# Kernel tuning notes

Hardware: AMD Instinct MI355X
Metric: run time of the kernel (lower is better)

The kernel has to match this reference:

```python
import jax, jax.numpy as jnp
import numpy as np

B, C, H, W = 8, 512, 32, 32
NUM_HEADS, D_K = 8, 64
EPS = 1e-5


def setup_inputs() -> dict:
    key = jax.random.key(0)
    ks = jax.random.split(key, 6)
    s = 1.0 / np.sqrt(C)
    return {
        "x": jax.random.normal(ks[0], (B, C, H, W), dtype=jnp.float32),
        "wq": jax.random.uniform(ks[1], (C, NUM_HEADS * D_K), jnp.float32, -s, s),
        "bq": jnp.zeros((NUM_HEADS * D_K,), jnp.float32),
        "wk": jax.random.uniform(ks[2], (C, NUM_HEADS * D_K), jnp.float32, -s, s),
        "bk": jnp.zeros((NUM_HEADS * D_K,), jnp.float32),
        "wv": jax.random.uniform(ks[3], (C, NUM_HEADS * D_K), jnp.float32, -s, s),
        "bv": jnp.zeros((NUM_HEADS * D_K,), jnp.float32),
        "ln_g": jnp.ones((C,), jnp.float32),
        "ln_b": jnp.zeros((C,), jnp.float32),
        "wo": jax.random.uniform(ks[4], (NUM_HEADS * D_K, C), jnp.float32, -s, s),
        "bo": jnp.zeros((C,), jnp.float32),
    }


def reference(x, wq, bq, wk, bk, wv, bv, ln_g, ln_b, wo, bo):
    b, c, h, w = x.shape
    seq = h * w
    # [B, C, H, W] -> [B, S, C]
    t = x.reshape(b, c, seq).transpose(0, 2, 1)
    residual = t
    # LayerNorm over channel dim
    mu = jnp.mean(t, axis=-1, keepdims=True)
    var = jnp.var(t, axis=-1, keepdims=True)
    tn = (t - mu) * jax.lax.rsqrt(var + EPS) * ln_g + ln_b
    # QKV projections -> [B, S, h, d]
    q = (tn @ wq + bq).reshape(b, seq, NUM_HEADS, D_K)
    k = (tn @ wk + bk).reshape(b, seq, NUM_HEADS, D_K)
    v = (tn @ wv + bv).reshape(b, seq, NUM_HEADS, D_K)
    scores = jnp.einsum("bqhd,bkhd->bhqk", q, k) / np.sqrt(D_K).astype(np.float32)
    attn = jax.nn.softmax(scores, axis=-1)
    out = jnp.einsum("bhqk,bkhd->bqhd", attn, v).reshape(b, seq, NUM_HEADS * D_K)
    out = out @ wo + bo
    return out + residual
```

## Files before the change

kernel.cpp:

```cpp
#include <hip/hip_runtime.h>
#include <hip/hip_bf16.h>
#include <stdint.h>

#define BB 8
#define CC 512
#define SS 1024
#define NH 8
#define DK 64
#define MM (BB*SS)
#define PQ 72

typedef __attribute__((ext_vector_type(8))) short bf16x8;
typedef __attribute__((ext_vector_type(4))) float f32x4;

__device__ inline float b2f(unsigned short u) {
    union { unsigned int i; float f; } x; x.i = ((unsigned int)u) << 16; return x.f;
}
__device__ inline unsigned short f2b(float f) {
    union { float f; unsigned int i; } x; x.f = f;
    unsigned int r = (x.i + 0x7FFFu + ((x.i >> 16) & 1u)) >> 16;
    return (unsigned short)r;
}
__device__ inline unsigned int cvtpk(float lo, float hi) {
    unsigned int r;
    asm("v_cvt_pk_bf16_f32 %0, %1, %2" : "=v"(r) : "v"(lo), "v"(hi));
    return r;
}
__device__ inline f32x4 mfma16(bf16x8 a, bf16x8 b, f32x4 c) {
    return __builtin_amdgcn_mfma_f32_16x16x32_bf16(a, b, c, 0, 0, 0);
}
__device__ __forceinline__ void gload16(const void* g, void* l) {
    __builtin_amdgcn_global_load_lds(
        (const __attribute__((address_space(1))) void*)g,
        (__attribute__((address_space(3))) void*)l, 16, 0, 0);
}

__global__ void __launch_bounds__(256) wtrans_kernel(const float* __restrict__ wq,
                                                     const float* __restrict__ wk,
                                                     const float* __restrict__ wv,
                                                     const float* __restrict__ wo,
                                                     unsigned short* __restrict__ wT) {
    __shared__ float lds[64][65];
    const float* w = (blockIdx.z == 0) ? wq : (blockIdx.z == 1) ? wk : (blockIdx.z == 2) ? wv : wo;
    unsigned short* o = wT + (size_t)blockIdx.z * (512 * 512);
    const int n0 = blockIdx.x * 64, k0 = blockIdx.y * 64;
    const int t = threadIdx.x;
    {
        const int nl = (t & 15) * 4, kr = t >> 4;
#pragma unroll
        for (int i = 0; i < 4; ++i) {
            float4 v = *(const float4*)(w + (size_t)(k0 + kr + i * 16) * 512 + n0 + nl);
            lds[kr + i * 16][nl] = v.x; lds[kr + i * 16][nl + 1] = v.y;
            lds[kr + i * 16][nl + 2] = v.z; lds[kr + i * 16][nl + 3] = v.w;
        }
    }
    __syncthreads();
    {
        const int k8 = (t & 7) * 8, nr = t >> 3;
#pragma unroll
        for (int ii = 0; ii < 2; ++ii) {
            int n = nr + ii * 32;
            unsigned short pk[8];
#pragma unroll
            for (int e = 0; e < 8; ++e) pk[e] = f2b(lds[k8 + e][n]);
            *(uint4*)&o[(size_t)(n0 + n) * 512 + k0 + k8] = *(uint4*)pk;
        }
    }
}

__global__ void __launch_bounds__(256) stats_kernel(const float* __restrict__ x,
                                                    float2* __restrict__ stats) {
    __shared__ float2 red[16][17];
    const int b = blockIdx.y, s0 = blockIdx.x * 16;
    const int sl = threadIdx.x & 15, cg = threadIdx.x >> 4;
    const float* xp = x + ((size_t)b * 512 + cg * 32) * 1024 + s0 + sl;
    float sum = 0.f, sq = 0.f;
#pragma unroll 8
    for (int i = 0; i < 32; ++i) { float v = xp[(size_t)i * 1024]; sum += v; sq += v * v; }
    red[cg][sl] = make_float2(sum, sq);
    __syncthreads();
    if (threadIdx.x < 16) {
        float s = 0.f, q = 0.f;
#pragma unroll
        for (int c = 0; c < 16; ++c) { s += red[c][threadIdx.x].x; q += red[c][threadIdx.x].y; }
        float mean = s * (1.f / 512.f);
        float var = q * (1.f / 512.f) - mean * mean;
        stats[b * 1024 + s0 + threadIdx.x] = make_float2(mean, rsqrtf(var + 1e-5f));
    }
}

__global__ void __launch_bounds__(256) xln_kernel(const float* __restrict__ x,
                                                  const float2* __restrict__ stats,
                                                  const float* __restrict__ g,
                                                  const float* __restrict__ bta,
                                                  unsigned short* __restrict__ xt,
                                                  unsigned short* __restrict__ tn) {
    __shared__ float lds[64][65];
    const int s0 = blockIdx.x * 64, c0 = blockIdx.y * 64, b = blockIdx.z;
    const int t = threadIdx.x;
    {
        const int sl = (t & 15) * 4, cr = t >> 4;
#pragma unroll
        for (int i = 0; i < 4; ++i) {
            float4 v = *(const float4*)(x + ((size_t)b * 512 + c0 + cr + i * 16) * 1024 + s0 + sl);
            lds[cr + i * 16][sl] = v.x; lds[cr + i * 16][sl + 1] = v.y;
            lds[cr + i * 16][sl + 2] = v.z; lds[cr + i * 16][sl + 3] = v.w;
        }
    }
    __syncthreads();
    {
        const int c8 = (t & 7) * 8, sr = t >> 3;
        float gg[8], bb[8];
        {
            float4 g0 = *(const float4*)(g + c0 + c8), g1 = *(const float4*)(g + c0 + c8 + 4);
            float4 b0 = *(const float4*)(bta + c0 + c8), b1 = *(const float4*)(bta + c0 + c8 + 4);
            gg[0]=g0.x; gg[1]=g0.y; gg[2]=g0.z; gg[3]=g0.w; gg[4]=g1.x; gg[5]=g1.y; gg[6]=g1.z; gg[7]=g1.w;
            bb[0]=b0.x; bb[1]=b0.y; bb[2]=b0.z; bb[3]=b0.w; bb[4]=b1.x; bb[5]=b1.y; bb[6]=b1.z; bb[7]=b1.w;
        }
#pragma unroll
        for (int ii = 0; ii < 2; ++ii) {
            int s = sr + ii * 32;
            float2 st = stats[b * 1024 + s0 + s];
            unsigned short rawp[8], nrmp[8];
#pragma unroll
            for (int e = 0; e < 8; ++e) {
                float v = lds[c8 + e][s];
                rawp[e] = f2b(v);
                nrmp[e] = f2b((v - st.x) * st.y * gg[e] + bb[e]);
            }
            *(uint4*)&xt[((size_t)b * 1024 + s0 + s) * 512 + c0 + c8] = *(uint4*)rawp;
            *(uint4*)&tn[((size_t)b * 1024 + s0 + s) * 512 + c0 + c8] = *(uint4*)nrmp;
        }
    }
}

__device__ inline void gemm_tile(const unsigned short* __restrict__ A,
                                 const unsigned short* __restrict__ Bt,
                                 int m0, int n0,
                                 unsigned short (*A_lds)[128 * 64],
                                 unsigned short (*B_lds)[128 * 64],
                                 f32x4 acc[4][4]) {
    const int t = threadIdx.x;
    const int lane = t & 63, w = t >> 6;
    const int l15 = lane & 15, l4 = lane >> 4;
    const int wm = (w >> 1) * 64, wn = (w & 1) * 64;
    auto STAGE = [&](int bi, int kt) {
#pragma unroll
        for (int i = 0; i < 4; ++i) {
            int chunk = i * 256 + t;
            int row = chunk >> 3, kc = (chunk & 7) * 8;
            gload16(A + (size_t)(m0 + row) * 512 + kt * 64 + kc, &A_lds[bi][chunk * 8]);
            gload16(Bt + (size_t)(n0 + row) * 512 + kt * 64 + kc, &B_lds[bi][chunk * 8]);
        }
    };
    STAGE(0, 0);
    __syncthreads();
#pragma unroll 1
    for (int kt = 0; kt < 8; ++kt) {
        const int bi = kt & 1;
        if (kt < 7) STAGE(bi ^ 1, kt + 1);
#pragma unroll
        for (int kk = 0; kk < 2; ++kk) {
            bf16x8 af[4], bfr[4];
#pragma unroll
            for (int i = 0; i < 4; ++i)
                af[i] = *(const bf16x8*)&A_lds[bi][(wm + i * 16 + l15) * 64 + kk * 32 + l4 * 8];
#pragma unroll
            for (int j = 0; j < 4; ++j)
                bfr[j] = *(const bf16x8*)&B_lds[bi][(wn + j * 16 + l15) * 64 + kk * 32 + l4 * 8];
#pragma unroll
            for (int i = 0; i < 4; ++i)
#pragma unroll
                for (int j = 0; j < 4; ++j)
                    acc[i][j] = mfma16(af[i], bfr[j], acc[i][j]);
        }
        __syncthreads();
    }
}

__global__ void __launch_bounds__(256) gemm_qkv_kernel(const unsigned short* __restrict__ tn,
                                                       const unsigned short* __restrict__ wT,
                                                       const float* __restrict__ bq,
                                                       const float* __restrict__ bk,
                                                       const float* __restrict__ bv,
                                                       unsigned short* __restrict__ outbase) {
    __shared__ alignas(16) unsigned short A_lds[2][128 * 64];
    __shared__ alignas(16) unsigned short B_lds[2][128 * 64];
    const int z = blockIdx.z;
    const unsigned short* Bt = wT + (size_t)z * (512 * 512);
    const float* bias = (z == 0) ? bq : (z == 1) ? bk : bv;
    const int m0 = blockIdx.x * 128, n0 = blockIdx.y * 128;
    f32x4 acc[4][4];
    const f32x4 z4 = {0.f, 0.f, 0.f, 0.f};
#pragma unroll
    for (int i = 0; i < 4; ++i)
#pragma unroll
        for (int j = 0; j < 4; ++j) acc[i][j] = z4;
    gemm_tile(tn, Bt, m0, n0, A_lds, B_lds, acc);
    const int lane = threadIdx.x & 63, w = threadIdx.x >> 6;
    const int l15 = lane & 15, l4 = lane >> 4;
    const int wm = (w >> 1) * 64, wn = (w & 1) * 64;
    if (z < 2) {
        unsigned short* out = outbase + (size_t)z * MM * 512;
#pragma unroll
        for (int i = 0; i < 4; ++i)
#pragma unroll
            for (int j = 0; j < 4; ++j) {
                int col = n0 + wn + j * 16 + l15;
                float bcol = bias[col];
#pragma unroll
                for (int r = 0; r < 4; ++r) {
                    int row = m0 + wm + i * 16 + l4 * 4 + r;
                    out[(size_t)row * 512 + col] = f2b(acc[i][j][r] + bcol);
                }
            }
    } else {
        unsigned short* vt = outbase + (size_t)2 * MM * 512;
#pragma unroll
        for (int i = 0; i < 4; ++i)
#pragma unroll
            for (int j = 0; j < 4; ++j) {
                int col = n0 + wn + j * 16 + l15;
                float bcol = bias[col];
                int rowb = m0 + wm + i * 16 + l4 * 4;
                int bi = rowb >> 10, s0 = rowb & 1023;
                uint2 pk;
                pk.x = (unsigned int)f2b(acc[i][j][0] + bcol) |
                       ((unsigned int)f2b(acc[i][j][1] + bcol) << 16);
                pk.y = (unsigned int)f2b(acc[i][j][2] + bcol) |
                       ((unsigned int)f2b(acc[i][j][3] + bcol) << 16);
                *(uint2*)&vt[((size_t)bi * 512 + col) * 1024 + s0] = pk;
            }
    }
}

__global__ void __launch_bounds__(256) attn_kernel(const unsigned short* __restrict__ q,
                                                   const unsigned short* __restrict__ k,
                                                   const unsigned short* __restrict__ vt,
                                                   unsigned short* __restrict__ o) {
    __shared__ alignas(16) unsigned short Kl[2][64 * 64];
    __shared__ alignas(16) unsigned short Vl[2][64 * 64];
    __shared__ alignas(16) unsigned short Pl[4][16 * PQ];
    const int qt = blockIdx.x, h = blockIdx.y, b = blockIdx.z;
    const int t = threadIdx.x, lane = t & 63, w = t >> 6;
    const int l15 = lane & 15, l4 = lane >> 4;

    const float QSC = 0.125f * 1.44269504f;
    const int qrow = qt * 64 + w * 16 + l15;
    const unsigned short* qp = q + ((size_t)(b * SS + qrow)) * 512 + h * 64;
    bf16x8 qf[2];
#pragma unroll
    for (int kk = 0; kk < 2; ++kk) {
        bf16x8 tmp = *(const bf16x8*)(qp + kk * 32 + l4 * 8);
#pragma unroll
        for (int e = 0; e < 8; ++e)
            tmp[e] = (short)f2b(b2f((unsigned short)tmp[e]) * QSC);
        qf[kk] = tmp;
    }

    const unsigned short* krow_base = k + ((size_t)(b * SS)) * 512 + h * 64;
    const unsigned short* vrow_base = vt + ((size_t)(b * NH + h) * DK) * SS;

    auto STAGE = [&](int bi, int kt) {
        const int key0 = kt * 64;
#pragma unroll
        for (int i = 0; i < 2; ++i) {
            int chunk = i * 256 + t;
            int row = chunk >> 3;
            int scb = ((chunk & 7) * 16) ^ ((row & 7) << 4);
            gload16((const char*)(krow_base + (size_t)(key0 + row) * 512) + scb,
                    &Kl[bi][chunk * 8]);
            gload16((const char*)(vrow_base + (size_t)row * SS + key0) + scb,
                    &Vl[bi][chunk * 8]);
        }
    };

    float m_run = -1e30f, l_run = 0.f;
    f32x4 acc_o[4];
    const f32x4 z4 = {0.f, 0.f, 0.f, 0.f};
#pragma unroll
    for (int j = 0; j < 4; ++j) acc_o[j] = z4;

    STAGE(0, 0);
    __syncthreads();

#pragma unroll 1
    for (int kt = 0; kt < 16; ++kt) {
        const int bi = kt & 1;
        if (kt < 15) STAGE(bi ^ 1, kt + 1);

        f32x4 sc[4];
#pragma unroll
        for (int j = 0; j < 4; ++j) sc[j] = z4;
        __builtin_amdgcn_s_setprio(1);
#pragma unroll
        for (int kk = 0; kk < 2; ++kk)
#pragma unroll
            for (int j = 0; j < 4; ++j) {
                int row = j * 16 + l15;
                int cb = (kk * 64 + l4 * 16) ^ ((row & 7) << 4);
                bf16x8 kf = *(const bf16x8*)((const char*)Kl[bi] + row * 128 + cb);
                sc[j] = mfma16(kf, qf[kk], sc[j]);
            }
        __builtin_amdgcn_s_setprio(0);

        float mx = fmaxf(fmaxf(sc[0][0], sc[0][1]), fmaxf(sc[0][2], sc[0][3]));
#pragma unroll
        for (int j = 1; j < 4; ++j)
            mx = fmaxf(mx, fmaxf(fmaxf(sc[j][0], sc[j][1]), fmaxf(sc[j][2], sc[j][3])));

        if (!__all(mx - m_run <= 8.f)) {
            mx = fmaxf(mx, __shfl_xor(mx, 16));
            mx = fmaxf(mx, __shfl_xor(mx, 32));
            float mnew = fmaxf(m_run, mx);
            float scl = exp2f(m_run - mnew);
            m_run = mnew;
            l_run *= scl;
            float scl_r[4];
#pragma unroll
            for (int r = 0; r < 4; ++r) scl_r[r] = __shfl(scl, (l4 << 2) | r);
#pragma unroll
            for (int j = 0; j < 4; ++j)
#pragma unroll
                for (int r = 0; r < 4; ++r) acc_o[j][r] *= scl_r[r];
        }

        float p[4][4], lsum = 0.f;
#pragma unroll
        for (int j = 0; j < 4; ++j)
#pragma unroll
            for (int r = 0; r < 4; ++r) {
                p[j][r] = exp2f(sc[j][r] - m_run);
                lsum += p[j][r];
            }
        l_run += lsum;

#pragma unroll
        for (int j = 0; j < 4; ++j) {
            uint2 pk;
            pk.x = cvtpk(p[j][0], p[j][1]);
            pk.y = cvtpk(p[j][2], p[j][3]);
            *(uint2*)&Pl[w][l15 * PQ + j * 16 + l4 * 4] = pk;
        }

        __builtin_amdgcn_s_setprio(1);
#pragma unroll
        for (int kk = 0; kk < 2; ++kk) {
            bf16x8 pf = *(const bf16x8*)&Pl[w][l15 * PQ + kk * 32 + l4 * 8];
#pragma unroll
            for (int j = 0; j < 4; ++j) {
                int row = j * 16 + l15;
                int cb = (kk * 64 + l4 * 16) ^ ((row & 7) << 4);
                bf16x8 vf = *(const bf16x8*)((const char*)Vl[bi] + row * 128 + cb);
                acc_o[j] = mfma16(pf, vf, acc_o[j]);
            }
        }
        __builtin_amdgcn_s_setprio(0);

        __syncthreads();
    }

    float l_tot = l_run;
    l_tot += __shfl_xor(l_tot, 16);
    l_tot += __shfl_xor(l_tot, 32);
    float l_r[4];
#pragma unroll
    for (int r = 0; r < 4; ++r) l_r[r] = __shfl(l_tot, (l4 << 2) | r);

#pragma unroll
    for (int j = 0; j < 4; ++j)
#pragma unroll
        for (int r = 0; r < 4; ++r) {
            int row = qt * 64 + w * 16 + l4 * 4 + r;
            float val = acc_o[j][r] / l_r[r];
            o[((size_t)(b * SS + row)) * 512 + h * 64 + j * 16 + l15] = f2b(val);
        }
}

__global__ void __launch_bounds__(256) gemm_out_kernel(const unsigned short* __restrict__ ao,
                                                       const unsigned short* __restrict__ woT,
                                                       const float* __restrict__ bo,
                                                       const unsigned short* __restrict__ xt,
                                                       float* __restrict__ out) {
    __shared__ alignas(16) unsigned short A_lds[2][128 * 64];
    __shared__ alignas(16) unsigned short B_lds[2][128 * 64];
    const int m0 = blockIdx.x * 128, n0 = blockIdx.y * 128;
    f32x4 acc[4][4];
    const f32x4 z4 = {0.f, 0.f, 0.f, 0.f};
#pragma unroll
    for (int i = 0; i < 4; ++i)
#pragma unroll
        for (int j = 0; j < 4; ++j) acc[i][j] = z4;
    gemm_tile(ao, woT, m0, n0, A_lds, B_lds, acc);
    const int lane = threadIdx.x & 63, w = threadIdx.x >> 6;
    const int l15 = lane & 15, l4 = lane >> 4;
    const int wm = (w >> 1) * 64, wn = (w & 1) * 64;
#pragma unroll
    for (int i = 0; i < 4; ++i)
#pragma unroll
        for (int j = 0; j < 4; ++j) {
            int col = n0 + wn + j * 16 + l15;
            float bcol = bo[col];
#pragma unroll
            for (int r = 0; r < 4; ++r) {
                int row = m0 + wm + i * 16 + l4 * 4 + r;
                float resid = b2f(xt[(size_t)row * 512 + col]);
                out[(size_t)row * 512 + col] = acc[i][j][r] + bcol + resid;
            }
        }
}

extern "C" void kernel_launch(void* const* d_in, const int* in_sizes, int n_in,
                              void* d_out, int out_size, void* d_ws, size_t ws_size,
                              hipStream_t stream) {
    const float* x   = (const float*)d_in[0];
    const float* wq  = (const float*)d_in[1];
    const float* bq  = (const float*)d_in[2];
    const float* wk  = (const float*)d_in[3];
    const float* bk  = (const float*)d_in[4];
    const float* wv  = (const float*)d_in[5];
    const float* bv  = (const float*)d_in[6];
    const float* lng = (const float*)d_in[7];
    const float* lnb = (const float*)d_in[8];
    const float* wo  = (const float*)d_in[9];
    const float* bo  = (const float*)d_in[10];
    float* out = (float*)d_out;

    unsigned short* ws  = (unsigned short*)d_ws;
    const size_t M1 = (size_t)1024 * 1024;
    unsigned short* tn   = ws;
    unsigned short* qkvb = ws + 4 * M1;
    unsigned short* wT   = ws + 16 * M1;
    unsigned short* xt   = ws + 17 * M1;
    unsigned short* ao   = tn;
    float2* stats = (float2*)qkvb;

    wtrans_kernel<<<dim3(8, 8, 4), 256, 0, stream>>>(wq, wk, wv, wo, wT);
    stats_kernel<<<dim3(64, 8), 256, 0, stream>>>(x, stats);
    xln_kernel<<<dim3(16, 8, 8), 256, 0, stream>>>(x, stats, lng, lnb, xt, tn);
    gemm_qkv_kernel<<<dim3(64, 4, 3), 256, 0, stream>>>(tn, wT, bq, bk, bv, qkvb);
    attn_kernel<<<dim3(16, 8, 8), 256, 0, stream>>>(qkvb,
                                                    qkvb + (size_t)MM * 512,
                                                    qkvb + (size_t)2 * MM * 512,
                                                    ao);
    gemm_out_kernel<<<dim3(64, 4), 256, 0, stream>>>(ao, wT + (size_t)3 * 512 * 512, bo, xt, out);
}
```

Baseline: 188.2 us.

## Load attention K/V fragments directly to registers, remap blocks to XCDs, vectorize stats

The attention kernel stops staging K and V tiles through shared memory with a block-wide barrier. Each wave now loads its own K and V MFMA fragments straight from global memory into registers and prefetches the next K tile. The grid is flattened and remapped so blocks sharing a batch/head land on the same XCD, aiming for better L2 reuse. The stats kernel uses float4 loads over 64 positions per block. In exchange, the four waves of a block each reload the same K/V data from global memory or cache, and register pressure rises.

After: 261.2 us. 38.8% more time.

```diff
diff --git a/kernel.cpp b/kernel.cpp
--- a/kernel.cpp
+++ b/kernel.cpp
@@ -70,16 +70,23 @@
 
 __global__ void __launch_bounds__(256) stats_kernel(const float* __restrict__ x,
                                                     float2* __restrict__ stats) {
-    __shared__ float2 red[16][17];
-    const int b = blockIdx.y, s0 = blockIdx.x * 16;
-    const int sl = threadIdx.x & 15, cg = threadIdx.x >> 4;
+    __shared__ float2 red[16][64];
+    const int b = blockIdx.y, s0 = blockIdx.x * 64;
+    const int sl = (threadIdx.x & 15) * 4, cg = threadIdx.x >> 4;
+    float sum[4] = {0.f, 0.f, 0.f, 0.f}, sq[4] = {0.f, 0.f, 0.f, 0.f};
     const float* xp = x + ((size_t)b * 512 + cg * 32) * 1024 + s0 + sl;
-    float sum = 0.f, sq = 0.f;
-#pragma unroll 8
-    for (int i = 0; i < 32; ++i) { float v = xp[(size_t)i * 1024]; sum += v; sq += v * v; }
-    red[cg][sl] = make_float2(sum, sq);
+#pragma unroll 4
+    for (int i = 0; i < 32; ++i) {
+        float4 v = *(const float4*)(xp + (size_t)i * 1024);
+        sum[0] += v.x; sq[0] += v.x * v.x;
+        sum[1] += v.y; sq[1] += v.y * v.y;
+        sum[2] += v.z; sq[2] += v.z * v.z;
+        sum[3] += v.w; sq[3] += v.w * v.w;
+    }
+#pragma unroll
+    for (int e = 0; e < 4; ++e) red[cg][sl + e] = make_float2(sum[e], sq[e]);
     __syncthreads();
-    if (threadIdx.x < 16) {
+    if (threadIdx.x < 64) {
         float s = 0.f, q = 0.f;
 #pragma unroll
         for (int c = 0; c < 16; ++c) { s += red[c][threadIdx.x].x; q += red[c][threadIdx.x].y; }
@@ -238,10 +245,10 @@
                                                    const unsigned short* __restrict__ k,
                                                    const unsigned short* __restrict__ vt,
                                                    unsigned short* __restrict__ o) {
-    __shared__ alignas(16) unsigned short Kl[2][64 * 64];
-    __shared__ alignas(16) unsigned short Vl[2][64 * 64];
     __shared__ alignas(16) unsigned short Pl[4][16 * PQ];
-    const int qt = blockIdx.x, h = blockIdx.y, b = blockIdx.z;
+    const int pid = blockIdx.x;
+    const int wgid = (pid & 7) * 128 + (pid >> 3);
+    const int qt = wgid & 15, h = (wgid >> 4) & 7, b = wgid >> 7;
     const int t = threadIdx.x, lane = t & 63, w = t >> 6;
     const int l15 = lane & 15, l4 = lane >> 4;
 
@@ -258,22 +265,8 @@
         qf[kk] = tmp;
     }
 
-    const unsigned short* krow_base = k + ((size_t)(b * SS)) * 512 + h * 64;
-    const unsigned short* vrow_base = vt + ((size_t)(b * NH + h) * DK) * SS;
-
-    auto STAGE = [&](int bi, int kt) {
-        const int key0 = kt * 64;
-#pragma unroll
-        for (int i = 0; i < 2; ++i) {
-            int chunk = i * 256 + t;
-            int row = chunk >> 3;
-            int scb = ((chunk & 7) * 16) ^ ((row & 7) << 4);
-            gload16((const char*)(krow_base + (size_t)(key0 + row) * 512) + scb,
-                    &Kl[bi][chunk * 8]);
-            gload16((const char*)(vrow_base + (size_t)row * SS + key0) + scb,
-                    &Vl[bi][chunk * 8]);
-        }
-    };
+    const unsigned short* kbase = k + ((size_t)(b * SS) + l15) * 512 + h * 64 + l4 * 8;
+    const unsigned short* vbase = vt + ((size_t)(b * NH + h) * DK + l15) * SS + l4 * 8;
 
     float m_run = -1e30f, l_run = 0.f;
     f32x4 acc_o[4];
@@ -281,13 +274,23 @@
 #pragma unroll
     for (int j = 0; j < 4; ++j) acc_o[j] = z4;
 
-    STAGE(0, 0);
-    __syncthreads();
-
-#pragma unroll 1
+    bf16x8 kf[2][4];
+#pragma unroll
+    for (int kk = 0; kk < 2; ++kk)
+#pragma unroll
+        for (int j = 0; j < 4; ++j)
+            kf[kk][j] = *(const bf16x8*)(kbase + (size_t)(j * 16) * 512 + kk * 32);
+
+#pragma unroll 2
     for (int kt = 0; kt < 16; ++kt) {
-        const int bi = kt & 1;
-        if (kt < 15) STAGE(bi ^ 1, kt + 1);
+        const int key0 = kt * 64;
+
+        bf16x8 vf[2][4];
+#pragma unroll
+        for (int kk = 0; kk < 2; ++kk)
+#pragma unroll
+            for (int j = 0; j < 4; ++j)
+                vf[kk][j] = *(const bf16x8*)(vbase + (size_t)(j * 16) * SS + key0 + kk * 32);
 
         f32x4 sc[4];
 #pragma unroll
@@ -296,13 +299,17 @@
 #pragma unroll
         for (int kk = 0; kk < 2; ++kk)
 #pragma unroll
-            for (int j = 0; j < 4; ++j) {
-                int row = j * 16 + l15;
-                int cb = (kk * 64 + l4 * 16) ^ ((row & 7) << 4);
-                bf16x8 kf = *(const bf16x8*)((const char*)Kl[bi] + row * 128 + cb);
-                sc[j] = mfma16(kf, qf[kk], sc[j]);
-            }
+            for (int j = 0; j < 4; ++j)
+                sc[j] = mfma16(kf[kk][j], qf[kk], sc[j]);
         __builtin_amdgcn_s_setprio(0);
+
+        const int keyn = (kt < 15) ? key0 + 64 : key0;
+        bf16x8 kn[2][4];
+#pragma unroll
+        for (int kk = 0; kk < 2; ++kk)
+#pragma unroll
+            for (int j = 0; j < 4; ++j)
+                kn[kk][j] = *(const bf16x8*)(kbase + (size_t)(keyn + j * 16) * 512 + kk * 32);
 
         float mx = fmaxf(fmaxf(sc[0][0], sc[0][1]), fmaxf(sc[0][2], sc[0][3]));
 #pragma unroll
@@ -348,16 +355,16 @@
         for (int kk = 0; kk < 2; ++kk) {
             bf16x8 pf = *(const bf16x8*)&Pl[w][l15 * PQ + kk * 32 + l4 * 8];
 #pragma unroll
-            for (int j = 0; j < 4; ++j) {
-                int row = j * 16 + l15;
-                int cb = (kk * 64 + l4 * 16) ^ ((row & 7) << 4);
-                bf16x8 vf = *(const bf16x8*)((const char*)Vl[bi] + row * 128 + cb);
-                acc_o[j] = mfma16(pf, vf, acc_o[j]);
-            }
+            for (int j = 0; j < 4; ++j)
+                acc_o[j] = mfma16(pf, vf[kk][j], acc_o[j]);
         }
         __builtin_amdgcn_s_setprio(0);
 
-        __syncthreads();
+#pragma unroll
+        for (int kk = 0; kk < 2; ++kk)
+#pragma unroll
+            for (int j = 0; j < 4; ++j)
+                kf[kk][j] = kn[kk][j];
     }
 
     float l_tot = l_run;
@@ -436,12 +443,12 @@
     float2* stats = (float2*)qkvb;
 
     wtrans_kernel<<<dim3(8, 8, 4), 256, 0, stream>>>(wq, wk, wv, wo, wT);
-    stats_kernel<<<dim3(64, 8), 256, 0, stream>>>(x, stats);
+    stats_kernel<<<dim3(16, 8), 256, 0, stream>>>(x, stats);
     xln_kernel<<<dim3(16, 8, 8), 256, 0, stream>>>(x, stats, lng, lnb, xt, tn);
     gemm_qkv_kernel<<<dim3(64, 4, 3), 256, 0, stream>>>(tn, wT, bq, bk, bv, qkvb);
-    attn_kernel<<<dim3(16, 8, 8), 256, 0, stream>>>(qkvb,
-                                                    qkvb + (size_t)MM * 512,
-                                                    qkvb + (size_t)2 * MM * 512,
-                                                    ao);
+    attn_kernel<<<1024, 256, 0, stream>>>(qkvb,
+                                          qkvb + (size_t)MM * 512,
+                                          qkvb + (size_t)2 * MM * 512,
+                                          ao);
     gemm_out_kernel<<<dim3(64, 4), 256, 0, stream>>>(ao, wT + (size_t)3 * 512 * 512, bo, xt, out);
 }
```

## Enlarge attention tiles to 128 queries per block and vectorize LN stats

Applied to the files above, without the earlier changes.

Attention blocks now use 8 waves covering 128 query rows, so each staged K/V tile is shared by twice as many queries. A remapped 1D grid groups blocks of the same batch/head. Staging is simplified to one 16-byte load per thread per tile. The online softmax always rescales instead of conditionally skipping it, and setprio hints are removed. The LayerNorm stats kernel uses float4 loads with 64 positions per block. The unconditional rescale adds per-iteration shuffle and multiply work.

After: 176.4 us. -6.3%, faster.

```diff
diff --git a/kernel.cpp b/kernel.cpp
--- a/kernel.cpp
+++ b/kernel.cpp
@@ -70,16 +70,23 @@
 
 __global__ void __launch_bounds__(256) stats_kernel(const float* __restrict__ x,
                                                     float2* __restrict__ stats) {
-    __shared__ float2 red[16][17];
-    const int b = blockIdx.y, s0 = blockIdx.x * 16;
-    const int sl = threadIdx.x & 15, cg = threadIdx.x >> 4;
+    __shared__ float2 red[16][64];
+    const int b = blockIdx.y, s0 = blockIdx.x * 64;
+    const int sl = (threadIdx.x & 15) * 4, cg = threadIdx.x >> 4;
+    float sum[4] = {0.f, 0.f, 0.f, 0.f}, sq[4] = {0.f, 0.f, 0.f, 0.f};
     const float* xp = x + ((size_t)b * 512 + cg * 32) * 1024 + s0 + sl;
-    float sum = 0.f, sq = 0.f;
-#pragma unroll 8
-    for (int i = 0; i < 32; ++i) { float v = xp[(size_t)i * 1024]; sum += v; sq += v * v; }
-    red[cg][sl] = make_float2(sum, sq);
+#pragma unroll 4
+    for (int i = 0; i < 32; ++i) {
+        float4 v = *(const float4*)(xp + (size_t)i * 1024);
+        sum[0] += v.x; sq[0] += v.x * v.x;
+        sum[1] += v.y; sq[1] += v.y * v.y;
+        sum[2] += v.z; sq[2] += v.z * v.z;
+        sum[3] += v.w; sq[3] += v.w * v.w;
+    }
+#pragma unroll
+    for (int e = 0; e < 4; ++e) red[cg][sl + e] = make_float2(sum[e], sq[e]);
     __syncthreads();
-    if (threadIdx.x < 16) {
+    if (threadIdx.x < 64) {
         float s = 0.f, q = 0.f;
 #pragma unroll
         for (int c = 0; c < 16; ++c) { s += red[c][threadIdx.x].x; q += red[c][threadIdx.x].y; }
@@ -234,19 +241,22 @@
     }
 }
 
-__global__ void __launch_bounds__(256) attn_kernel(const unsigned short* __restrict__ q,
+__global__ void __launch_bounds__(512) attn_kernel(const unsigned short* __restrict__ q,
                                                    const unsigned short* __restrict__ k,
                                                    const unsigned short* __restrict__ vt,
                                                    unsigned short* __restrict__ o) {
     __shared__ alignas(16) unsigned short Kl[2][64 * 64];
     __shared__ alignas(16) unsigned short Vl[2][64 * 64];
-    __shared__ alignas(16) unsigned short Pl[4][16 * PQ];
-    const int qt = blockIdx.x, h = blockIdx.y, b = blockIdx.z;
+    __shared__ alignas(16) unsigned short Pl[8][16 * PQ];
+    const int pid = blockIdx.x;
+    const int g = (pid >> 6) * 8 + (pid & 7);
+    const int qt = (pid >> 3) & 7;
+    const int b = g >> 3, h = g & 7;
     const int t = threadIdx.x, lane = t & 63, w = t >> 6;
     const int l15 = lane & 15, l4 = lane >> 4;
 
     const float QSC = 0.125f * 1.44269504f;
-    const int qrow = qt * 64 + w * 16 + l15;
+    const int qrow = qt * 128 + w * 16 + l15;
     const unsigned short* qp = q + ((size_t)(b * SS + qrow)) * 512 + h * 64;
     bf16x8 qf[2];
 #pragma unroll
@@ -258,22 +268,10 @@
         qf[kk] = tmp;
     }
 
-    const unsigned short* krow_base = k + ((size_t)(b * SS)) * 512 + h * 64;
-    const unsigned short* vrow_base = vt + ((size_t)(b * NH + h) * DK) * SS;
-
-    auto STAGE = [&](int bi, int kt) {
-        const int key0 = kt * 64;
-#pragma unroll
-        for (int i = 0; i < 2; ++i) {
-            int chunk = i * 256 + t;
-            int row = chunk >> 3;
-            int scb = ((chunk & 7) * 16) ^ ((row & 7) << 4);
-            gload16((const char*)(krow_base + (size_t)(key0 + row) * 512) + scb,
-                    &Kl[bi][chunk * 8]);
-            gload16((const char*)(vrow_base + (size_t)row * SS + key0) + scb,
-                    &Vl[bi][chunk * 8]);
-        }
-    };
+    const int srow = t >> 3;
+    const int scb = ((t & 7) * 16) ^ ((srow & 7) << 4);
+    const char* kptr = (const char*)(k + ((size_t)(b * SS) + srow) * 512 + h * 64) + scb;
+    const char* vptr = (const char*)(vt + ((size_t)(b * NH + h) * DK + srow) * SS) + scb;
 
     float m_run = -1e30f, l_run = 0.f;
     f32x4 acc_o[4];
@@ -281,18 +279,25 @@
 #pragma unroll
     for (int j = 0; j < 4; ++j) acc_o[j] = z4;
 
-    STAGE(0, 0);
+    gload16(kptr, &Kl[0][t * 8]);
+    gload16(vptr, &Vl[0][t * 8]);
+    kptr += 64 * 512 * 2;
+    vptr += 64 * 2;
     __syncthreads();
 
 #pragma unroll 1
     for (int kt = 0; kt < 16; ++kt) {
         const int bi = kt & 1;
-        if (kt < 15) STAGE(bi ^ 1, kt + 1);
+        if (kt < 15) {
+            gload16(kptr, &Kl[bi ^ 1][t * 8]);
+            gload16(vptr, &Vl[bi ^ 1][t * 8]);
+            kptr += 64 * 512 * 2;
+            vptr += 64 * 2;
+        }
 
         f32x4 sc[4];
 #pragma unroll
         for (int j = 0; j < 4; ++j) sc[j] = z4;
-        __builtin_amdgcn_s_setprio(1);
 #pragma unroll
         for (int kk = 0; kk < 2; ++kk)
 #pragma unroll
@@ -302,38 +307,26 @@
                 bf16x8 kf = *(const bf16x8*)((const char*)Kl[bi] + row * 128 + cb);
                 sc[j] = mfma16(kf, qf[kk], sc[j]);
             }
-        __builtin_amdgcn_s_setprio(0);
 
         float mx = fmaxf(fmaxf(sc[0][0], sc[0][1]), fmaxf(sc[0][2], sc[0][3]));
 #pragma unroll
         for (int j = 1; j < 4; ++j)
             mx = fmaxf(mx, fmaxf(fmaxf(sc[j][0], sc[j][1]), fmaxf(sc[j][2], sc[j][3])));
-
-        if (!__all(mx - m_run <= 8.f)) {
-            mx = fmaxf(mx, __shfl_xor(mx, 16));
-            mx = fmaxf(mx, __shfl_xor(mx, 32));
-            float mnew = fmaxf(m_run, mx);
-            float scl = exp2f(m_run - mnew);
-            m_run = mnew;
-            l_run *= scl;
-            float scl_r[4];
-#pragma unroll
-            for (int r = 0; r < 4; ++r) scl_r[r] = __shfl(scl, (l4 << 2) | r);
-#pragma unroll
-            for (int j = 0; j < 4; ++j)
-#pragma unroll
-                for (int r = 0; r < 4; ++r) acc_o[j][r] *= scl_r[r];
-        }
+        mx = fmaxf(mx, __shfl_xor(mx, 16));
+        mx = fmaxf(mx, __shfl_xor(mx, 32));
+        const float mnew = fmaxf(m_run, mx);
+        const float scl = exp2f(m_run - mnew);
+        m_run = mnew;
 
         float p[4][4], lsum = 0.f;
 #pragma unroll
         for (int j = 0; j < 4; ++j)
 #pragma unroll
             for (int r = 0; r < 4; ++r) {
-                p[j][r] = exp2f(sc[j][r] - m_run);
+                p[j][r] = exp2f(sc[j][r] - mnew);
                 lsum += p[j][r];
             }
-        l_run += lsum;
+        l_run = l_run * scl + lsum;
 
 #pragma unroll
         for (int j = 0; j < 4; ++j) {
@@ -343,7 +336,14 @@
             *(uint2*)&Pl[w][l15 * PQ + j * 16 + l4 * 4] = pk;
         }
 
-        __builtin_amdgcn_s_setprio(1);
+        float scl_r[4];
+#pragma unroll
+        for (int r = 0; r < 4; ++r) scl_r[r] = __shfl(scl, (l4 << 2) | r);
+#pragma unroll
+        for (int j = 0; j < 4; ++j)
+#pragma unroll
+            for (int r = 0; r < 4; ++r) acc_o[j][r] *= scl_r[r];
+
 #pragma unroll
         for (int kk = 0; kk < 2; ++kk) {
             bf16x8 pf = *(const bf16x8*)&Pl[w][l15 * PQ + kk * 32 + l4 * 8];
@@ -355,7 +355,6 @@
                 acc_o[j] = mfma16(pf, vf, acc_o[j]);
             }
         }
-        __builtin_amdgcn_s_setprio(0);
 
         __syncthreads();
     }
@@ -371,7 +370,7 @@
     for (int j = 0; j < 4; ++j)
 #pragma unroll
         for (int r = 0; r < 4; ++r) {
-            int row = qt * 64 + w * 16 + l4 * 4 + r;
+            int row = qt * 128 + w * 16 + l4 * 4 + r;
             float val = acc_o[j][r] / l_r[r];
             o[((size_t)(b * SS + row)) * 512 + h * 64 + j * 16 + l15] = f2b(val);
         }
@@ -436,12 +435,12 @@
     float2* stats = (float2*)qkvb;
 
     wtrans_kernel<<<dim3(8, 8, 4), 256, 0, stream>>>(wq, wk, wv, wo, wT);
-    stats_kernel<<<dim3(64, 8), 256, 0, stream>>>(x, stats);
+    stats_kernel<<<dim3(16, 8), 256, 0, stream>>>(x, stats);
     xln_kernel<<<dim3(16, 8, 8), 256, 0, stream>>>(x, stats, lng, lnb, xt, tn);
     gemm_qkv_kernel<<<dim3(64, 4, 3), 256, 0, stream>>>(tn, wT, bq, bk, bv, qkvb);
-    attn_kernel<<<dim3(16, 8, 8), 256, 0, stream>>>(qkvb,
-                                                    qkvb + (size_t)MM * 512,
-                                                    qkvb + (size_t)2 * MM * 512,
-                                                    ao);
+    attn_kernel<<<512, 512, 0, stream>>>(qkvb,
+                                         qkvb + (size_t)MM * 512,
+                                         qkvb + (size_t)2 * MM * 512,
+                                         ao);
     gemm_out_kernel<<<dim3(64, 4), 256, 0, stream>>>(ao, wT + (size_t)3 * 512 * 512, bo, xt, out);
 }
```
